# Optimization experiments

Measured on AMD Instinct MI355X. Metric: run time of the kernel, lower is better.

Reference implementation:

```python
import jax, jax.numpy as jnp
import numpy as np


def _butter1(Wn, highpass):
    """First-order Butterworth digital coefficients (bilinear transform),
    matching scipy.signal.butter(1, Wn, btype). Wn is nyquist-normalized."""
    K = jnp.tan(jnp.pi * Wn / 2.0)
    a1 = (K - 1.0) / (K + 1.0)
    if highpass:
        b0 = 1.0 / (K + 1.0)
        b1 = -b0
    else:
        b0 = K / (K + 1.0)
        b1 = b0
    return b0, b1, a1


def setup_inputs() -> dict:
    key = jax.random.key(0)
    B, T = 128, 262144
    x = jax.random.normal(key, (B, T), dtype=jnp.float32)
    return {
        "x": x,
        "center_freq": jnp.float32(1000.0),  # nn.Parameter
        "bandwidth": jnp.float32(500.0),     # nn.Parameter
        "gain": jnp.float32(1.0),            # nn.Parameter
        "sample_rate": 48000,
    }


def reference(x, center_freq, bandwidth, gain, sample_rate):
    nyq = sample_rate / 2.0
    low_wn = (center_freq - bandwidth / 2.0) / nyq
    high_wn = (center_freq + bandwidth / 2.0) / nyq
    # cascaded 1st-order highpass(low_wn) then lowpass(high_wn) = bandpass
    bh0, bh1, ah1 = _butter1(low_wn, highpass=True)
    bl0, bl1, al1 = _butter1(high_wn, highpass=False)

    xt = x.T  # [T, B] -- scan over time, vectorized over batch
    zeros = jnp.zeros((x.shape[0],), dtype=x.dtype)

    def step(carry, x_t):
        x_prev, y1_prev, y2_prev = carry
        y1 = bh0 * x_t + bh1 * x_prev - ah1 * y1_prev   # highpass stage
        y2 = bl0 * y1 + bl1 * y1_prev - al1 * y2_prev   # lowpass stage
        return (x_t, y1, y2), y2

    _, yt = jax.lax.scan(step, (zeros, zeros, zeros), xt)
    return yt.T * gain  # [B, T]
```

## Files before the change

### kernel.cpp

```cpp
#include <hip/hip_runtime.h>
#include <math.h>

#define B_    128
#define T_    262144
#define L_    32
#define NT_   256
#define WCH_  8
#define OT_   (NT_ * L_)
#define TPR_  (T_ / OT_)
#define STR_  (L_ + 1)
#define NCH_  (NT_ + WCH_)

struct Coef {
    float bh0, bh1;
    float p, q, r;
    float blc0, blc1;
};

__device__ inline Coef compute_coefs(float cf, float bw, int sr) {
    const float PIH = 1.57079632679489661923f;
    float nyq = 0.5f * (float)sr;
    float low_wn  = (cf - 0.5f * bw) / nyq;
    float high_wn = (cf + 0.5f * bw) / nyq;
    float K1 = tanf(PIH * low_wn);
    float K2 = tanf(PIH * high_wn);
    Coef c;
    float inv1 = 1.0f / (K1 + 1.0f);
    c.bh0 = inv1;
    c.bh1 = -inv1;
    float ah1 = (K1 - 1.0f) * inv1;
    float inv2 = 1.0f / (K2 + 1.0f);
    float bl0 = K2 * inv2;
    float al1 = (K2 - 1.0f) * inv2;
    c.p = -ah1;
    c.r = -al1;
    c.q = bl0 - bl0 * ah1;
    c.blc0 = bl0 * c.bh0;
    c.blc1 = bl0 * c.bh1;
    return c;
}

__device__ inline void iir_step(const Coef& c, float xt, float& x_prev,
                                float& y1, float& y2) {
    float c1 = fmaf(c.bh0,  xt, c.bh1  * x_prev);
    float cx = fmaf(c.blc0, xt, c.blc1 * x_prev);
    float ny1 = fmaf(c.p, y1, c1);
    float ny2 = fmaf(c.q, y1, fmaf(c.r, y2, cx));
    y1 = ny1; y2 = ny2; x_prev = xt;
}

struct Mat { float p, q, r; };
__device__ inline Mat mat_sq(Mat m) {
    Mat o; o.p = m.p * m.p; o.q = m.q * (m.p + m.r); o.r = m.r * m.r; return o;
}
__device__ inline Mat mat_mul(Mat a, Mat b) {
    Mat o; o.p = a.p * b.p; o.q = fmaf(a.q, b.p, a.r * b.q); o.r = a.r * b.r;
    return o;
}
__device__ inline float2 mat_apply_add(Mat m, float2 v, float2 add) {
    float2 o;
    o.x = fmaf(m.p, v.x, add.x);
    o.y = fmaf(m.q, v.x, fmaf(m.r, v.y, add.y));
    return o;
}

__global__ __launch_bounds__(256) void bp_kernel(
        const float* __restrict__ x, float* __restrict__ out,
        const float* __restrict__ cfp, const float* __restrict__ bwp,
        const float* __restrict__ gp, const int* __restrict__ srp) {
    __shared__ float xs[NCH_ * STR_];
    __shared__ float2 ks[NT_];
    __shared__ float2 wagg[WCH_];

    const int blk = blockIdx.x;
    const int row = blk >> 5;
    const int ti  = blk & (TPR_ - 1);
    const int t   = threadIdx.x;
    const Coef cf = compute_coefs(*cfp, *bwp, *srp);
    const float gain = *gp;
    const long tile_start = (long)row * T_ + (long)ti * OT_;

    if (t < 64) {
        float4 v = make_float4(0.f, 0.f, 0.f, 0.f);
        if (ti != 0) v = ((const float4*)(x + tile_start - WCH_ * L_))[t];
        int chunk = t >> 3, pos = (4 * t) & 31;
        float* p = xs + chunk * STR_ + pos;
        p[0] = v.x; p[1] = v.y; p[2] = v.z; p[3] = v.w;
    }
    const float4* xg = (const float4*)(x + tile_start);
    #pragma unroll
    for (int k = 0; k < 8; ++k) {
        int F = t + NT_ * k;
        float4 v = xg[F];
        int g = WCH_ * L_ + 4 * F;
        int chunk = g >> 5, pos = g & 31;
        float* p = xs + chunk * STR_ + pos;
        p[0] = v.x; p[1] = v.y; p[2] = v.z; p[3] = v.w;
    }
    __syncthreads();

    float y2l[L_];
    float y1 = 0.f, y2 = 0.f;
    {
        int k = WCH_ + t;
        float x_prev = xs[(k - 1) * STR_ + (L_ - 1)];
        const float* cp = xs + k * STR_;
        #pragma unroll
        for (int i = 0; i < L_; ++i) {
            iir_step(cf, cp[i], x_prev, y1, y2);
            y2l[i] = y2;
        }
    }
    ks[t] = make_float2(y1, y2);

    if ((t & 31) == 0) {
        int j = t >> 5;
        float wy1 = 0.f, wy2 = 0.f;
        float wxp = (j == 0) ? 0.0f : xs[(j - 1) * STR_ + (L_ - 1)];
        const float* cp = xs + j * STR_;
        #pragma unroll
        for (int i = 0; i < L_; ++i) iir_step(cf, cp[i], wxp, wy1, wy2);
        wagg[j] = make_float2(wy1, wy2);
    }
    __syncthreads();

    Mat A  = { cf.p, cf.q, cf.r };
    Mat AL = A;
    #pragma unroll
    for (int k = 0; k < 5; ++k) AL = mat_sq(AL);
    float2 s0 = make_float2(0.f, 0.f);
    #pragma unroll
    for (int j = 0; j < WCH_; ++j) s0 = mat_apply_add(AL, s0, wagg[j]);

    float2 a = make_float2(y1, y2);
    Mat Pw = AL;
    for (int o = 1; o < NT_; o <<= 1) {
        float2 v = (t >= o) ? ks[t - o] : make_float2(0.f, 0.f);
        __syncthreads();
        if (t >= o) a = mat_apply_add(Pw, v, a);
        ks[t] = a;
        __syncthreads();
        Pw = mat_sq(Pw);
    }
    float2 e = (t > 0) ? ks[t - 1] : make_float2(0.f, 0.f);

    Mat R = { 1.f, 0.f, 1.f };
    Mat Mp = AL;
    unsigned tt = (unsigned)t;
    #pragma unroll
    for (int k = 0; k < 8; ++k) {
        if (tt & 1u) R = mat_mul(Mp, R);
        tt >>= 1;
        if (k < 7) Mp = mat_sq(Mp);
    }
    float2 E = mat_apply_add(R, s0, e);

    float c1 = E.x, c2 = E.y;
    {
        float* cp = xs + (WCH_ + t) * STR_;
        #pragma unroll
        for (int i = 0; i < L_; ++i) {
            float nc1 = cf.p * c1;
            float nc2 = fmaf(cf.q, c1, cf.r * c2);
            c1 = nc1; c2 = nc2;
            cp[i] = (y2l[i] + c2) * gain;
        }
    }
    __syncthreads();

    float4* og = (float4*)(out + tile_start);
    #pragma unroll
    for (int k = 0; k < 8; ++k) {
        int F = t + NT_ * k;
        int g = WCH_ * L_ + 4 * F;
        int chunk = g >> 5, pos = g & 31;
        const float* p = xs + chunk * STR_ + pos;
        og[F] = make_float4(p[0], p[1], p[2], p[3]);
    }
}

extern "C" void kernel_launch(void* const* d_in, const int* in_sizes, int n_in,
                              void* d_out, int out_size, void* d_ws, size_t ws_size,
                              hipStream_t stream) {
    const float* x   = (const float*)d_in[0];
    const float* cfp = (const float*)d_in[1];
    const float* bwp = (const float*)d_in[2];
    const float* gp  = (const float*)d_in[3];
    const int*   srp = (const int*)d_in[4];
    float* out = (float*)d_out;

    dim3 blk(NT_), grd(B_ * TPR_);
    bp_kernel<<<grd, blk, 0, stream>>>(x, out, cfp, bwp, gp, srp);
}
```

Before: 240.6 us.

## Replace LDS block scan with wave shuffles, halve chunk length, compute coefs once

```diff
diff --git a/kernel.cpp b/kernel.cpp
--- a/kernel.cpp
+++ b/kernel.cpp
@@ -3,42 +3,20 @@
 
 #define B_    128
 #define T_    262144
-#define L_    32
+#define L_    16
 #define NT_   256
-#define WCH_  8
+#define WCH_  16
 #define OT_   (NT_ * L_)
 #define TPR_  (T_ / OT_)
 #define STR_  (L_ + 1)
 #define NCH_  (NT_ + WCH_)
+#define NW_   (NT_ / 64)
 
 struct Coef {
     float bh0, bh1;
     float p, q, r;
     float blc0, blc1;
 };
-
-__device__ inline Coef compute_coefs(float cf, float bw, int sr) {
-    const float PIH = 1.57079632679489661923f;
-    float nyq = 0.5f * (float)sr;
-    float low_wn  = (cf - 0.5f * bw) / nyq;
-    float high_wn = (cf + 0.5f * bw) / nyq;
-    float K1 = tanf(PIH * low_wn);
-    float K2 = tanf(PIH * high_wn);
-    Coef c;
-    float inv1 = 1.0f / (K1 + 1.0f);
-    c.bh0 = inv1;
-    c.bh1 = -inv1;
-    float ah1 = (K1 - 1.0f) * inv1;
-    float inv2 = 1.0f / (K2 + 1.0f);
-    float bl0 = K2 * inv2;
-    float al1 = (K2 - 1.0f) * inv2;
-    c.p = -ah1;
-    c.r = -al1;
-    c.q = bl0 - bl0 * ah1;
-    c.blc0 = bl0 * c.bh0;
-    c.blc1 = bl0 * c.bh1;
-    return c;
-}
 
 __device__ inline void iir_step(const Coef& c, float xt, float& x_prev,
                                 float& y1, float& y2) {
@@ -64,40 +42,66 @@
     return o;
 }
 
-__global__ __launch_bounds__(256) void bp_kernel(
+__global__ __launch_bounds__(NT_, 8) void bp_kernel(
         const float* __restrict__ x, float* __restrict__ out,
         const float* __restrict__ cfp, const float* __restrict__ bwp,
         const float* __restrict__ gp, const int* __restrict__ srp) {
     __shared__ float xs[NCH_ * STR_];
-    __shared__ float2 ks[NT_];
     __shared__ float2 wagg[WCH_];
-
-    const int blk = blockIdx.x;
-    const int row = blk >> 5;
-    const int ti  = blk & (TPR_ - 1);
-    const int t   = threadIdx.x;
-    const Coef cf = compute_coefs(*cfp, *bwp, *srp);
-    const float gain = *gp;
+    __shared__ float2 wsagg[NW_];
+    __shared__ float cbuf[8];
+
+    const int blk  = blockIdx.x;
+    const int row  = blk >> 6;
+    const int ti   = blk & (TPR_ - 1);
+    const int t    = threadIdx.x;
+    const int lane = t & 63;
+    const int wav  = t >> 6;
     const long tile_start = (long)row * T_ + (long)ti * OT_;
+
+    if (t == 0) {
+        const float PIH = 1.57079632679489661923f;
+        float cfv = *cfp, bwv = *bwp;
+        float nyq = 0.5f * (float)(*srp);
+        float K1 = tanf(PIH * (cfv - 0.5f * bwv) / nyq);
+        float K2 = tanf(PIH * (cfv + 0.5f * bwv) / nyq);
+        float inv1 = 1.0f / (K1 + 1.0f);
+        float ah1 = (K1 - 1.0f) * inv1;
+        float inv2 = 1.0f / (K2 + 1.0f);
+        float bl0 = K2 * inv2;
+        float al1 = (K2 - 1.0f) * inv2;
+        cbuf[0] = inv1;
+        cbuf[1] = -inv1;
+        cbuf[2] = -ah1;
+        cbuf[3] = bl0 - bl0 * ah1;
+        cbuf[4] = -al1;
+        cbuf[5] = bl0 * inv1;
+        cbuf[6] = -bl0 * inv1;
+        cbuf[7] = *gp;
+    }
 
     if (t < 64) {
         float4 v = make_float4(0.f, 0.f, 0.f, 0.f);
         if (ti != 0) v = ((const float4*)(x + tile_start - WCH_ * L_))[t];
-        int chunk = t >> 3, pos = (4 * t) & 31;
+        int chunk = t >> 2, pos = 4 * (t & 3);
         float* p = xs + chunk * STR_ + pos;
         p[0] = v.x; p[1] = v.y; p[2] = v.z; p[3] = v.w;
     }
     const float4* xg = (const float4*)(x + tile_start);
     #pragma unroll
-    for (int k = 0; k < 8; ++k) {
+    for (int k = 0; k < 4; ++k) {
         int F = t + NT_ * k;
         float4 v = xg[F];
-        int g = WCH_ * L_ + 4 * F;
-        int chunk = g >> 5, pos = g & 31;
+        int chunk = WCH_ + (F >> 2), pos = 4 * (F & 3);
         float* p = xs + chunk * STR_ + pos;
         p[0] = v.x; p[1] = v.y; p[2] = v.z; p[3] = v.w;
     }
     __syncthreads();
+
+    Coef cf;
+    cf.bh0 = cbuf[0]; cf.bh1 = cbuf[1]; cf.p = cbuf[2]; cf.q = cbuf[3];
+    cf.r = cbuf[4]; cf.blc0 = cbuf[5]; cf.blc1 = cbuf[6];
+    const float gain = cbuf[7];
 
     float y2l[L_];
     float y1 = 0.f, y2 = 0.f;
@@ -111,52 +115,60 @@
             y2l[i] = y2;
         }
     }
-    ks[t] = make_float2(y1, y2);
-
-    if ((t & 31) == 0) {
-        int j = t >> 5;
+
+    if (t < WCH_) {
         float wy1 = 0.f, wy2 = 0.f;
-        float wxp = (j == 0) ? 0.0f : xs[(j - 1) * STR_ + (L_ - 1)];
-        const float* cp = xs + j * STR_;
+        float wxp = (t == 0) ? 0.0f : xs[(t - 1) * STR_ + (L_ - 1)];
+        const float* cp = xs + t * STR_;
         #pragma unroll
         for (int i = 0; i < L_; ++i) iir_step(cf, cp[i], wxp, wy1, wy2);
-        wagg[j] = make_float2(wy1, wy2);
-    }
-    __syncthreads();
+        wagg[t] = make_float2(wy1, wy2);
+    }
 
     Mat A  = { cf.p, cf.q, cf.r };
     Mat AL = A;
     #pragma unroll
-    for (int k = 0; k < 5; ++k) AL = mat_sq(AL);
-    float2 s0 = make_float2(0.f, 0.f);
-    #pragma unroll
-    for (int j = 0; j < WCH_; ++j) s0 = mat_apply_add(AL, s0, wagg[j]);
+    for (int k = 0; k < 4; ++k) AL = mat_sq(AL);
 
     float2 a = make_float2(y1, y2);
     Mat Pw = AL;
-    for (int o = 1; o < NT_; o <<= 1) {
-        float2 v = (t >= o) ? ks[t - o] : make_float2(0.f, 0.f);
-        __syncthreads();
-        if (t >= o) a = mat_apply_add(Pw, v, a);
-        ks[t] = a;
-        __syncthreads();
+    #pragma unroll
+    for (int o = 1; o < 64; o <<= 1) {
+        float vx = __shfl_up(a.x, (unsigned)o, 64);
+        float vy = __shfl_up(a.y, (unsigned)o, 64);
+        if (lane >= o) {
+            a.y = fmaf(Pw.q, vx, fmaf(Pw.r, vy, a.y));
+            a.x = fmaf(Pw.p, vx, a.x);
+        }
         Pw = mat_sq(Pw);
     }
-    float2 e = (t > 0) ? ks[t - 1] : make_float2(0.f, 0.f);
+    float2 ex;
+    ex.x = __shfl_up(a.x, 1u, 64);
+    ex.y = __shfl_up(a.y, 1u, 64);
+    if (lane == 0) { ex.x = 0.f; ex.y = 0.f; }
+    if (lane == 63) wsagg[wav] = a;
+    __syncthreads();
+
+    float2 S = make_float2(0.f, 0.f);
+    #pragma unroll
+    for (int j = 0; j < WCH_; ++j) S = mat_apply_add(AL, S, wagg[j]);
+    #pragma unroll
+    for (int u = 0; u < NW_ - 1; ++u)
+        if (wav > u) S = mat_apply_add(Pw, S, wsagg[u]);
 
     Mat R = { 1.f, 0.f, 1.f };
     Mat Mp = AL;
-    unsigned tt = (unsigned)t;
-    #pragma unroll
-    for (int k = 0; k < 8; ++k) {
-        if (tt & 1u) R = mat_mul(Mp, R);
-        tt >>= 1;
-        if (k < 7) Mp = mat_sq(Mp);
-    }
-    float2 E = mat_apply_add(R, s0, e);
-
-    float c1 = E.x, c2 = E.y;
+    unsigned b = (unsigned)lane;
+    #pragma unroll
+    for (int k = 0; k < 6; ++k) {
+        if (b & 1u) R = mat_mul(Mp, R);
+        b >>= 1u;
+        if (k < 5) Mp = mat_sq(Mp);
+    }
+    float2 E = mat_apply_add(R, S, ex);
+
     {
+        float c1 = E.x, c2 = E.y;
         float* cp = xs + (WCH_ + t) * STR_;
         #pragma unroll
         for (int i = 0; i < L_; ++i) {
@@ -170,10 +182,9 @@
 
     float4* og = (float4*)(out + tile_start);
     #pragma unroll
-    for (int k = 0; k < 8; ++k) {
+    for (int k = 0; k < 4; ++k) {
         int F = t + NT_ * k;
-        int g = WCH_ * L_ + 4 * F;
-        int chunk = g >> 5, pos = g & 31;
+        int chunk = WCH_ + (F >> 2), pos = 4 * (F & 3);
         const float* p = xs + chunk * STR_ + pos;
         og[F] = make_float4(p[0], p[1], p[2], p[3]);
     }
```

Result: no change. 239.4 us (-0.5%).
